# Performance work log

Measured on AMD Instinct MI355X. Metric: run time of the kernel, lower is better.

Reference implementation:

```python
import jax, jax.numpy as jnp
import numpy as np

T, S, B, D, H, F, E = 1024, 1024, 4, 1024, 16, 4096, 8
HD = D // H
N = T * B                      # tokens entering MoE
CAP = 2 * N // E               # top-2 capacity per expert


def setup_inputs() -> dict:
    key = jax.random.key(0)
    ks = jax.random.split(key, 16)
    sc = 0.02
    rn = lambda k, shp, s=sc: jax.random.normal(k, shp, jnp.float32) * s
    return {
        "tgt": jax.random.normal(ks[0], (T, B, D), jnp.float32),
        "memory": jax.random.normal(ks[1], (S, B, D), jnp.float32),
        "sa_in_w": rn(ks[2], (3 * D, D)), "sa_in_b": jnp.zeros((3 * D,), jnp.float32),
        "sa_out_w": rn(ks[3], (D, D)), "sa_out_b": jnp.zeros((D,), jnp.float32),
        "ca_in_w": rn(ks[4], (3 * D, D)), "ca_in_b": jnp.zeros((3 * D,), jnp.float32),
        "ca_out_w": rn(ks[5], (D, D)), "ca_out_b": jnp.zeros((D,), jnp.float32),
        "ln1_g": jnp.ones((D,), jnp.float32), "ln1_b": jnp.zeros((D,), jnp.float32),
        "ln2_g": jnp.ones((D,), jnp.float32), "ln2_b": jnp.zeros((D,), jnp.float32),
        "ln3_g": jnp.ones((D,), jnp.float32), "ln3_b": jnp.zeros((D,), jnp.float32),
        "wg": rn(ks[6], (D, E)),
        "w1": rn(ks[7], (E, D, F)), "b1": jnp.zeros((E, F), jnp.float32),
        "w2": rn(ks[8], (E, F, D)), "b2": jnp.zeros((E, D), jnp.float32),
    }


def layer_norm(x, g, b, eps=1e-5):
    mu = jnp.mean(x, axis=-1, keepdims=True)
    var = jnp.var(x, axis=-1, keepdims=True)
    return (x - mu) * jax.lax.rsqrt(var + eps) * g + b


def mha(q_in, k_in, v_in, in_w, in_b, out_w, out_b):
    # q_in: [Tq,B,D], k_in/v_in: [Tk,B,D]; torch MultiheadAttention math (eval)
    wq, wk, wv = jnp.split(in_w, 3, axis=0)
    bq, bk, bv = jnp.split(in_b, 3)
    def heads(x, w, bias):
        y = x @ w.T + bias                       # [Tx,B,D]
        return y.reshape(x.shape[0], B, H, HD).transpose(1, 2, 0, 3)  # [B,H,Tx,hd]
    q, k, v = heads(q_in, wq, bq), heads(k_in, wk, bk), heads(v_in, wv, bv)
    scores = jnp.einsum('bhtd,bhsd->bhts', q, k) / np.sqrt(HD)
    attn = jax.nn.softmax(scores, axis=-1)
    o = jnp.einsum('bhts,bhsd->bhtd', attn, v)   # [B,H,Tq,hd]
    o = o.transpose(2, 0, 1, 3).reshape(q_in.shape[0], B, D)
    return o @ out_w.T + out_b


def moe_top2(x, wg, w1, b1, w2, b2):
    # x: [N,D]. Top-2 gating with capacity dispatch + grouped expert FFN.
    logits = x @ wg                               # [N,E]
    gates = jax.nn.softmax(logits, axis=-1)
    idx1 = jnp.argmax(gates, axis=-1)             # [N]
    m1 = jax.nn.one_hot(idx1, E, dtype=x.dtype)   # [N,E]
    gates_wo1 = jnp.where(m1 > 0, -jnp.inf, logits)
    idx2 = jnp.argmax(gates_wo1, axis=-1)
    m2 = jax.nn.one_hot(idx2, E, dtype=x.dtype)
    ar = jnp.arange(N)
    g1 = gates[ar, idx1]
    g2 = gates[ar, idx2]
    denom = g1 + g2 + 1e-9
    g1, g2 = g1 / denom, g2 / denom
    # positions within each expert buffer (first-come-first-serve, top1 before top2)
    pos1 = jnp.cumsum(m1, axis=0)[ar, idx1] - 1
    counts1 = jnp.sum(m1, axis=0)                 # [E]
    pos2 = jnp.cumsum(m2, axis=0)[ar, idx2] - 1 + counts1[idx2]
    keep1 = (pos1 < CAP).astype(x.dtype)
    keep2 = (pos2 < CAP).astype(x.dtype)
    p1 = jnp.clip(pos1, 0, CAP - 1).astype(jnp.int32)
    p2 = jnp.clip(pos2, 0, CAP - 1).astype(jnp.int32)
    buf = jnp.zeros((E, CAP, D), x.dtype)
    buf = buf.at[idx1, p1].add(x * keep1[:, None])
    buf = buf.at[idx2, p2].add(x * keep2[:, None])
    # grouped expert FFN: [E,CAP,D] -> [E,CAP,F] -> [E,CAP,D]
    h = jax.nn.relu(jnp.einsum('ecd,edf->ecf', buf, w1) + b1[:, None, :])
    eo = jnp.einsum('ecf,efd->ecd', h, w2) + b2[:, None, :]
    out = eo[idx1, p1] * (g1 * keep1)[:, None] + eo[idx2, p2] * (g2 * keep2)[:, None]
    return out


def reference(tgt, memory, sa_in_w, sa_in_b, sa_out_w, sa_out_b,
              ca_in_w, ca_in_b, ca_out_w, ca_out_b,
              ln1_g, ln1_b, ln2_g, ln2_b, ln3_g, ln3_b,
              wg, w1, b1, w2, b2):
    t2 = mha(tgt, tgt, tgt, sa_in_w, sa_in_b, sa_out_w, sa_out_b)
    x = layer_norm(tgt + t2, ln1_g, ln1_b)
    t2 = mha(x, memory, memory, ca_in_w, ca_in_b, ca_out_w, ca_out_b)
    x = layer_norm(x + t2, ln2_g, ln2_b)
    m = moe_top2(x.reshape(N, D), wg, w1, b1, w2, b2).reshape(T, B, D)
    x = layer_norm(x + m, ln3_g, ln3_b)
    return x
```

## Files before the change

### kernel.cpp

```cpp
#include <hip/hip_runtime.h>
#include <hip/hip_bf16.h>


typedef __bf16 bf16;
typedef __bf16 bf16x2 __attribute__((ext_vector_type(2)));
typedef __bf16 bf16x4 __attribute__((ext_vector_type(4)));
typedef __bf16 bf16x8 __attribute__((ext_vector_type(8)));
typedef float  f32x4  __attribute__((ext_vector_type(4)));

static_assert(sizeof(bf16) == 2, "bf16 size");

#define CAP_ 1024

#define GLOAD16(g, l)                                                  \
  __builtin_amdgcn_global_load_lds(                                    \
      (const __attribute__((address_space(1))) unsigned int*)(g),      \
      (__attribute__((address_space(3))) unsigned int*)(l), 16, 0, 0)

#define BAR() do { asm volatile("" ::: "memory"); __builtin_amdgcn_s_barrier(); asm volatile("" ::: "memory"); } while (0)

static const long OFF_WSAIN  = 0L;
static const long OFF_WSAOUT = 6291456L;
static const long OFF_WCAIN  = 8388608L;
static const long OFF_WCAOUT = 14680064L;
static const long OFF_BTGT   = 16777216L;
static const long OFF_BMEM   = 25165824L;
static const long OFF_QKV    = 33554432L;
static const long OFF_QS     = OFF_QKV;
static const long OFF_KS     = OFF_QKV + 8388608L;
static const long OFF_VS     = OFF_QKV + 16777216L;
static const long OFF_EO1    = 33554432L;
static const long OFF_VT     = 58720256L;
static const long OFF_AO     = 67108864L;
static const long OFF_PROJ   = 75497472L;
static const long OFF_X1     = 92274688L;
static const long OFF_X2     = 109051904L;
static const long OFF_SCORES = 125829120L;
static const long OFF_H      = OFF_SCORES + 67108864L;
static const long OFF_GATE   = 260046848L;
static const long OFF_E1   = OFF_GATE;
static const long OFF_E2   = OFF_GATE + 16384L;
static const long OFF_G1   = OFF_GATE + 32768L;
static const long OFF_G2   = OFF_GATE + 49152L;
static const long OFF_D1   = OFF_GATE + 65536L;
static const long OFF_D2   = OFF_GATE + 81920L;
static const long OFF_S1   = OFF_GATE + 98304L;
static const long OFF_S2   = OFF_GATE + 114688L;

__device__ __forceinline__ int xcd_swz(int bid, int nwg) {
  int q = nwg >> 3, r = nwg & 7;
  int xcd = bid & 7, idx = bid >> 3;
  return (xcd < r ? xcd * (q + 1) : r * (q + 1) + (xcd - r) * q) + idx;
}

__global__ __launch_bounds__(256) void k_cvt6(
    const float* __restrict__ s0, const float* __restrict__ s1,
    const float* __restrict__ s2, const float* __restrict__ s3,
    const float* __restrict__ s4, const float* __restrict__ s5,
    bf16* __restrict__ d0, bf16* __restrict__ d1, bf16* __restrict__ d2,
    bf16* __restrict__ d3, bf16* __restrict__ d4, bf16* __restrict__ d5) {
  long b = blockIdx.x;
  const float* s; bf16* d; long off;
  if (b < 3072)       { s = s0; d = d0; off = b; }
  else if (b < 4096)  { s = s1; d = d1; off = b - 3072; }
  else if (b < 7168)  { s = s2; d = d2; off = b - 4096; }
  else if (b < 8192)  { s = s3; d = d3; off = b - 7168; }
  else if (b < 12288) { s = s4; d = d4; off = b - 8192; }
  else                { s = s5; d = d5; off = b - 12288; }
  long i = off * 256 + threadIdx.x;
  float4 v = ((const float4*)s)[i];
  bf16x4 o = {(bf16)v.x, (bf16)v.y, (bf16)v.z, (bf16)v.w};
  ((bf16x4*)d)[i] = o;
}

__global__ __launch_bounds__(256) void k_transpose_f32_bf16(const float* __restrict__ in,
                                                            bf16* __restrict__ out, int R, int C) {
  __shared__ float t[64][66];
  int z = blockIdx.z;
  long r0 = (long)blockIdx.y * 64, c0 = (long)blockIdx.x * 64;
  const float* ib = in + (long)z * R * C;
  bf16* ob = out + (long)z * R * C;
  int tid = threadIdx.x;
  int x = tid & 15, y = tid >> 4;
  #pragma unroll
  for (int j = 0; j < 4; j++) {
    int sr = y + j * 16;
    float4 v = *(const float4*)&ib[(r0 + sr) * C + c0 + x * 4];
    t[sr][x * 4 + 0] = v.x; t[sr][x * 4 + 1] = v.y;
    t[sr][x * 4 + 2] = v.z; t[sr][x * 4 + 3] = v.w;
  }
  __syncthreads();
  int xs = tid & 7, jj = tid >> 3;
  #pragma unroll
  for (int p = 0; p < 2; p++) {
    int c = jj + p * 32;
    bf16x8 o;
    #pragma unroll
    for (int k = 0; k < 8; k++) o[k] = (bf16)t[xs * 8 + k][c];
    *(bf16x8*)&ob[(c0 + c) * R + r0 + xs * 8] = o;
  }
}

__global__ __launch_bounds__(256) void k_extract_vt(const bf16* __restrict__ in,
                                                    bf16* __restrict__ out) {
  __shared__ bf16 t[64][68];
  const int bh = blockIdx.y;
  const long r0 = (long)blockIdx.x * 64;
  const int b = bh >> 4, h = bh & 15;
  const bf16* ib = in + (long)b * 1048576 + h * 64;
  bf16* ob = out + (long)bh * 65536;
  int tid = threadIdx.x;
  int x = tid & 15, y = tid >> 4;
  #pragma unroll
  for (int j = 0; j < 4; j++) {
    int sr = y + j * 16;
    *(bf16x4*)&t[sr][x * 4] = *(const bf16x4*)&ib[(r0 + sr) * 1024 + x * 4];
  }
  __syncthreads();
  #pragma unroll
  for (int p = 0; p < 4; p++) {
    int c = y + p * 16;
    bf16x4 o = {t[x * 4 + 0][c], t[x * 4 + 1][c], t[x * 4 + 2][c], t[x * 4 + 3][c]};
    *(bf16x4*)&ob[(long)c * 1024 + r0 + x * 4] = o;
  }
}

template <int BM, int BN, int WM, int WN, bool RELU, bool PERM, typename OutT>
__global__ __launch_bounds__(256) void k_gemm_nt(
    const bf16* __restrict__ A, const bf16* __restrict__ Bp,
    OutT* __restrict__ C, const float* __restrict__ bias,
    int K, long lda, long ldb, long ldc, float alpha, int zdiv,
    long sA1, long sA0, long sB1, long sB0, long sC1, long sC0,
    long sBias1, long sBias0) {
  constexpr int BK = 32;
  constexpr int WTM = BM / WM, WTN = BN / WN, MR = WTM / 16, NR = WTN / 16;
  constexpr int AISS = BM * BK / 2048;
  constexpr int BISS = BN * BK / 2048;
  __shared__ bf16 sa[BM * BK];
  __shared__ bf16 sb[BN * BK];
  const int nwg = gridDim.x * gridDim.y * gridDim.z;
  const int bid = blockIdx.x + gridDim.x * (blockIdx.y + gridDim.y * blockIdx.z);
  const int lid = xcd_swz(bid, nwg);
  const int bx = lid % gridDim.x;
  const int rem = lid / gridDim.x;
  const int by = rem % gridDim.y;
  const int z = rem / gridDim.y;
  const int zh = z / zdiv, zl = z - zh * zdiv;
  const bf16* Ab = A + zh * sA1 + zl * sA0 + (long)by * BM * lda;
  const bf16* Bb = Bp + zh * sB1 + zl * sB0 + (long)bx * BN * ldb;
  const int tid = threadIdx.x, lane = tid & 63, wid = tid >> 6;
  const int wm = wid / WN, wn = wid % WN;

  const int srow = tid >> 2;
  const int scol = (tid & 3) * 8;
  const bf16* aptr[AISS];
  bf16* aldst[AISS];
  #pragma unroll
  for (int i = 0; i < AISS; i++) {
    aptr[i] = Ab + (long)(srow + i * 64) * lda + scol;
    aldst[i] = &sa[i * 2048 + (wid << 9)];
  }
  const bf16* bptr[BISS];
  bf16* bldst[BISS];
  #pragma unroll
  for (int i = 0; i < BISS; i++) {
    bptr[i] = Bb + (long)(srow + i * 64) * ldb + scol;
    bldst[i] = &sb[i * 2048 + (wid << 9)];
  }

  f32x4 acc[MR][NR] = {};
  const int rA = wm * WTM + (lane & 15);
  const int rB = wn * WTN + (lane & 15);
  const int kk = (lane >> 4) * 8;

  for (int k0 = 0; k0 < K; k0 += BK) {
    #pragma unroll
    for (int i = 0; i < AISS; i++) GLOAD16(aptr[i] + k0, aldst[i]);
    #pragma unroll
    for (int i = 0; i < BISS; i++) GLOAD16(bptr[i] + k0, bldst[i]);
    __syncthreads();
    bf16x8 af[MR], bfr[NR];
    #pragma unroll
    for (int mi = 0; mi < MR; mi++) af[mi] = *(const bf16x8*)&sa[(rA + mi * 16) * BK + kk];
    #pragma unroll
    for (int ni = 0; ni < NR; ni++) bfr[ni] = *(const bf16x8*)&sb[(rB + ni * 16) * BK + kk];
    #pragma unroll
    for (int mi = 0; mi < MR; mi++)
      #pragma unroll
      for (int ni = 0; ni < NR; ni++)
        acc[mi][ni] = __builtin_amdgcn_mfma_f32_16x16x32_bf16(af[mi], bfr[ni], acc[mi][ni], 0, 0, 0);
    __syncthreads();
  }
  OutT* Cb = C + zh * sC1 + zl * sC0;
  const float* biasb = bias ? (bias + zh * sBias1 + zl * sBias0) : nullptr;
  const long rowBase = (long)by * BM + wm * WTM + ((lane >> 4) * 4);
  const long colBase = (long)bx * BN + wn * WTN + (lane & 15);
  #pragma unroll
  for (int mi = 0; mi < MR; mi++) {
    #pragma unroll
    for (int ni = 0; ni < NR; ni++) {
      long col = colBase + ni * 16;
      float bv = biasb ? biasb[col] : 0.f;
      #pragma unroll
      for (int r = 0; r < 4; r++) {
        long row = rowBase + mi * 16 + r;
        long prow = PERM ? ((row & 3) * 1024 + (row >> 2)) : row;
        float v = acc[mi][ni][r] * alpha + bv;
        if (RELU) v = fmaxf(v, 0.f);
        Cb[prow * ldc + col] = (OutT)v;
      }
    }
  }
}

template <bool RELU, bool PERM, typename OutT>
__global__ __launch_bounds__(512, 2) void k_gemm8p(
    const bf16* __restrict__ A, const bf16* __restrict__ Bp,
    OutT* __restrict__ C, const float* __restrict__ bias,
    int K, long lda, long ldb, long ldc, int zdiv,
    long sA1, long sA0, long sB1, long sB0, long sC1, long sC0, long sBias1) {
  __shared__ bf16 smem[65536];
  const int nwg = gridDim.x * gridDim.y * gridDim.z;
  const int bid = blockIdx.x + gridDim.x * (blockIdx.y + gridDim.y * blockIdx.z);
  const int lid = xcd_swz(bid, nwg);
  const int bx = lid % gridDim.x;
  const int rem = lid / gridDim.x;
  const int by = rem % gridDim.y;
  const int z = rem / gridDim.y;
  const int zh = z / zdiv, zl = z - zh * zdiv;
  const bf16* Ab = A + zh * sA1 + zl * sA0 + (long)by * 256 * lda;
  const bf16* Bb = Bp + zh * sB1 + zl * sB0 + (long)bx * 256 * ldb;
  const int tid = threadIdx.x, lane = tid & 63, wid = tid >> 6;
  const int wm = wid >> 2, wn = wid & 3;
  const int lane15 = lane & 15, grp = lane >> 4;
  const int s_r = (wid << 3) + (lane >> 3);
  const int s_k = ((lane & 7) ^ (lane >> 3)) << 3;
  const int ldst = wid << 9;
  const int in0 = (grp << 4) ^ ((lane & 7) << 4);
  const int in1 = (64 | (grp << 4)) ^ ((lane & 7) << 4);

  const int NT = K >> 6;
  f32x4 acc[8][4] = {};
  bf16x8 a[4][2], b[2][2][2];

  const bf16* pA0 = Ab + (long)s_r * lda + s_k;
  const bf16* pB0 = Bb + (long)s_r * ldb + s_k;

  auto stageA = [&](int q, long koff, int cb) {
    GLOAD16(pA0 + (long)(q << 6) * lda + koff, &smem[cb + (q << 12) + ldst]);
  };
  auto stageB = [&](int q, long koff, int cb) {
    GLOAD16(pB0 + (long)(q << 6) * ldb + koff, &smem[cb + 16384 + (q << 12) + ldst]);
  };
  auto loadA_ks = [&](int mh, int ks, int cb) {
    const int inx = ks ? in1 : in0;
    #pragma unroll
    for (int mi2 = 0; mi2 < 4; mi2++) {
      int r = wm * 128 + mh * 64 + mi2 * 16 + lane15;
      a[mi2][ks] = *(const bf16x8*)&smem[cb + (r << 6) + (inx >> 1)];
    }
  };
  auto loadB_ks = [&](int nh, int ks, int cb) {
    const int inx = ks ? in1 : in0;
    #pragma unroll
    for (int ni2 = 0; ni2 < 2; ni2++) {
      int c = wn * 64 + nh * 32 + ni2 * 16 + lane15;
      b[nh][ni2][ks] = *(const bf16x8*)&smem[cb + 16384 + (c << 6) + (inx >> 1)];
    }
  };
  auto mfmaQ = [&](int mh, int nh) {
    __builtin_amdgcn_s_setprio(1);
    #pragma unroll
    for (int ks = 0; ks < 2; ks++)
      #pragma unroll
      for (int mi2 = 0; mi2 < 4; mi2++)
        #pragma unroll
        for (int ni2 = 0; ni2 < 2; ni2++)
          acc[mh * 4 + mi2][nh * 2 + ni2] = __builtin_amdgcn_mfma_f32_16x16x32_bf16(
              a[mi2][ks], b[nh][ni2][ks], acc[mh * 4 + mi2][nh * 2 + ni2], 0, 0, 0);
    __builtin_amdgcn_s_setprio(0);
  };

  #pragma unroll
  for (int q = 0; q < 4; q++) { stageA(q, 0, 0); stageB(q, 0, 0); }
  #pragma unroll
  for (int q = 0; q < 4; q++) { stageA(q, 64, 32768); stageB(q, 64, 32768); }
  asm volatile("s_waitcnt vmcnt(8)" ::: "memory");
  BAR();
  loadB_ks(0, 0, 0);
  loadB_ks(0, 1, 0);

  long koff = 128;
  for (int t = 0; t < NT; t++) {
    const int cb = (t & 1) << 15;
    const bool dostage = (t + 2) < NT;
    const bool doread = (t + 1) < NT;
    loadA_ks(0, 0, cb);
    BAR();
    loadA_ks(0, 1, cb);
    loadB_ks(1, 0, cb);
    loadB_ks(1, 1, cb);
    mfmaQ(0, 0);
    BAR();
    if (dostage) { stageA(0, koff, cb); stageA(2, koff, cb); }
    BAR();
    mfmaQ(0, 1);
    BAR();
    loadA_ks(1, 0, cb);
    if (dostage) {
      stageB(0, koff, cb); stageB(1, koff, cb);
      stageB(2, koff, cb); stageB(3, koff, cb);
    }
    BAR();
    loadA_ks(1, 1, cb);
    mfmaQ(1, 0);
    BAR();
    if (dostage) {
      stageA(1, koff, cb); stageA(3, koff, cb);
      asm volatile("s_waitcnt vmcnt(8)" ::: "memory");
    } else if (doread) {
      asm volatile("s_waitcnt vmcnt(0)" ::: "memory");
    }
    BAR();
    if (doread) {
      loadB_ks(0, 0, cb ^ 32768);
      loadB_ks(0, 1, cb ^ 32768);
    }
    mfmaQ(1, 1);
    BAR();
    koff += 64;
  }

  OutT* Cb = C + zh * sC1 + zl * sC0;
  const float* biasb = bias ? (bias + zh * sBias1) : nullptr;
  float bv[4];
  #pragma unroll
  for (int ni = 0; ni < 4; ni++)
    bv[ni] = biasb ? biasb[(long)bx * 256 + wn * 64 + ni * 16 + lane15] : 0.f;
  const long rowBase = (long)by * 256 + wm * 128 + grp * 4;
  const long colBase = (long)bx * 256 + wn * 64 + lane15;
  #pragma unroll
  for (int mi = 0; mi < 8; mi++) {
    #pragma unroll
    for (int ni = 0; ni < 4; ni++) {
      long col = colBase + ni * 16;
      #pragma unroll
      for (int r = 0; r < 4; r++) {
        long row = rowBase + mi * 16 + r;
        long prow = PERM ? ((row & 3) * 1024 + (row >> 2)) : row;
        float v = acc[mi][ni][r] + bv[ni];
        if (RELU) v = fmaxf(v, 0.f);
        Cb[prow * ldc + col] = (OutT)v;
      }
    }
  }
}

__global__ __launch_bounds__(256) void k_flash(
    const bf16* __restrict__ q, const bf16* __restrict__ kk,
    const bf16* __restrict__ vt, bf16* __restrict__ ao) {
  __shared__ bf16 kt[2][2048];
  __shared__ bf16 vtt[2][2048];
  __shared__ bf16 p_lds[4][32 * 72];
  const int nwg = gridDim.x * gridDim.y;
  const int bid = blockIdx.x + gridDim.x * blockIdx.y;
  const int lid = xcd_swz(bid, nwg);
  const int qt = lid & 7;
  const int bh = lid >> 3;
  const int b = bh >> 4, h = bh & 15;
  const int tid = threadIdx.x, lane = tid & 63, wid = tid >> 6;
  const int colLane = lane & 15, grp = lane >> 4;
  const bf16* qb = q + (long)b * 1048576 + h * 64;
  const bf16* kb = kk + (long)b * 1048576 + h * 64;
  const bf16* vb = vt + (long)bh * 65536;

  bf16x8 qf[2][2];
  const int qrow0 = qt * 128 + wid * 32 + colLane;
  #pragma unroll
  for (int mi = 0; mi < 2; mi++)
    #pragma unroll
    for (int ks = 0; ks < 2; ks++)
      qf[mi][ks] = *(const bf16x8*)&qb[(long)(qrow0 + mi * 16) * 1024 + ks * 32 + grp * 8];

  const int srow = tid >> 2;
  const int scol = (tid & 3) * 8;

  f32x4 oacc[2][4] = {};
  float m_[2][4], l_[2][4];
  #pragma unroll
  for (int mi = 0; mi < 2; mi++)
    #pragma unroll
    for (int r = 0; r < 4; r++) { m_[mi][r] = -INFINITY; l_[mi][r] = 0.f; }
  bf16* pl = &p_lds[wid][0];

  for (int s0 = 0; s0 < 1024; s0 += 64) {
    GLOAD16(&kb[(long)(s0 + srow) * 1024 + scol], &kt[0][wid << 9]);
    GLOAD16(&kb[(long)(s0 + srow) * 1024 + 32 + scol], &kt[1][wid << 9]);
    GLOAD16(&vb[(long)srow * 1024 + s0 + scol], &vtt[0][wid << 9]);
    GLOAD16(&vb[(long)srow * 1024 + s0 + 32 + scol], &vtt[1][wid << 9]);
    __syncthreads();

    f32x4 sacc[2][4] = {};
    bf16x8 kf[4][2];
    #pragma unroll
    for (int ni = 0; ni < 4; ni++)
      #pragma unroll
      for (int ks = 0; ks < 2; ks++)
        kf[ni][ks] = *(const bf16x8*)&kt[ks][(colLane + ni * 16) * 32 + grp * 8];
    #pragma unroll
    for (int ks = 0; ks < 2; ks++)
      #pragma unroll
      for (int mi = 0; mi < 2; mi++)
        #pragma unroll
        for (int ni = 0; ni < 4; ni++)
          sacc[mi][ni] = __builtin_amdgcn_mfma_f32_16x16x32_bf16(qf[mi][ks], kf[ni][ks], sacc[mi][ni], 0, 0, 0);

    float mnew[2][4], sc[2][4], psum[2][4];
    #pragma unroll
    for (int mi = 0; mi < 2; mi++)
      #pragma unroll
      for (int r = 0; r < 4; r++) {
        float vx = fmaxf(fmaxf(sacc[mi][0][r], sacc[mi][1][r]),
                         fmaxf(sacc[mi][2][r], sacc[mi][3][r])) * 0.125f;
        #pragma unroll
        for (int o = 1; o < 16; o <<= 1) vx = fmaxf(vx, __shfl_xor(vx, o));
        float mn = fmaxf(m_[mi][r], vx);
        sc[mi][r] = __expf(m_[mi][r] - mn);
        m_[mi][r] = mn; mnew[mi][r] = mn;
        l_[mi][r] *= sc[mi][r];
        psum[mi][r] = 0.f;
      }
    #pragma unroll
    for (int mi = 0; mi < 2; mi++)
      #pragma unroll
      for (int ni = 0; ni < 4; ni++)
        #pragma unroll
        for (int r = 0; r < 4; r++)
          oacc[mi][ni][r] *= sc[mi][r];
    #pragma unroll
    for (int mi = 0; mi < 2; mi++)
      #pragma unroll
      for (int ni = 0; ni < 4; ni++)
        #pragma unroll
        for (int r = 0; r < 4; r++) {
          float p = __expf(sacc[mi][ni][r] * 0.125f - mnew[mi][r]);
          psum[mi][r] += p;
          pl[(mi * 16 + grp * 4 + r) * 72 + ni * 16 + colLane] = (bf16)p;
        }
    #pragma unroll
    for (int mi = 0; mi < 2; mi++)
      #pragma unroll
      for (int r = 0; r < 4; r++) {
        float ps = psum[mi][r];
        #pragma unroll
        for (int o = 1; o < 16; o <<= 1) ps += __shfl_xor(ps, o);
        l_[mi][r] += ps;
      }

    bf16x8 pa[2][2], vf[4][2];
    #pragma unroll
    for (int mi = 0; mi < 2; mi++)
      #pragma unroll
      for (int ks = 0; ks < 2; ks++)
        pa[mi][ks] = *(const bf16x8*)&pl[(colLane + mi * 16) * 72 + ks * 32 + grp * 8];
    #pragma unroll
    for (int ni = 0; ni < 4; ni++)
      #pragma unroll
      for (int ks = 0; ks < 2; ks++)
        vf[ni][ks] = *(const bf16x8*)&vtt[ks][(colLane + ni * 16) * 32 + grp * 8];
    #pragma unroll
    for (int ks = 0; ks < 2; ks++)
      #pragma unroll
      for (int mi = 0; mi < 2; mi++)
        #pragma unroll
        for (int ni = 0; ni < 4; ni++)
          oacc[mi][ni] = __builtin_amdgcn_mfma_f32_16x16x32_bf16(pa[mi][ks], vf[ni][ks], oacc[mi][ni], 0, 0, 0);
    __syncthreads();
  }

  #pragma unroll
  for (int mi = 0; mi < 2; mi++)
    #pragma unroll
    for (int r = 0; r < 4; r++) {
      float inv = 1.f / l_[mi][r];
      int t = qt * 128 + wid * 32 + mi * 16 + grp * 4 + r;
      long n = (long)t * 4 + b;
      #pragma unroll
      for (int ni = 0; ni < 4; ni++)
        ao[n * 1024 + h * 64 + ni * 16 + colLane] = (bf16)(oacc[mi][ni][r] * inv);
    }
}

__global__ __launch_bounds__(256) void k_add_ln(const float* __restrict__ a, const float* __restrict__ b,
                                                const float* __restrict__ g, const float* __restrict__ be,
                                                float* __restrict__ out, bf16* __restrict__ outb) {
  long row = blockIdx.x;
  int tid = threadIdx.x;
  float4 va = ((const float4*)(a + row * 1024))[tid];
  float4 vb = ((const float4*)(b + row * 1024))[tid];
  float v[4] = {va.x + vb.x, va.y + vb.y, va.z + vb.z, va.w + vb.w};
  float s = v[0] + v[1] + v[2] + v[3];
  float sq = v[0] * v[0] + v[1] * v[1] + v[2] * v[2] + v[3] * v[3];
  #pragma unroll
  for (int o = 32; o; o >>= 1) { s += __shfl_xor(s, o); sq += __shfl_xor(sq, o); }
  __shared__ float r1[4], r2[4];
  int wid = tid >> 6;
  if ((tid & 63) == 0) { r1[wid] = s; r2[wid] = sq; }
  __syncthreads();
  s = r1[0] + r1[1] + r1[2] + r1[3];
  sq = r2[0] + r2[1] + r2[2] + r2[3];
  float mu = s * (1.f / 1024.f);
  float var = sq * (1.f / 1024.f) - mu * mu;
  float rstd = rsqrtf(var + 1e-5f);
  float4 vg = ((const float4*)g)[tid];
  float4 vbe = ((const float4*)be)[tid];
  float y0 = (v[0] - mu) * rstd * vg.x + vbe.x;
  float y1 = (v[1] - mu) * rstd * vg.y + vbe.y;
  float y2 = (v[2] - mu) * rstd * vg.z + vbe.z;
  float y3 = (v[3] - mu) * rstd * vg.w + vbe.w;
  ((float4*)(out + row * 1024))[tid] = make_float4(y0, y1, y2, y3);
  if (outb) {
    bf16x4 o = {(bf16)y0, (bf16)y1, (bf16)y2, (bf16)y3};
    ((bf16x4*)(outb + row * 1024))[tid] = o;
  }
}

__global__ __launch_bounds__(256) void k_add_ln_gate(
    const float* __restrict__ a, const float* __restrict__ b,
    const float* __restrict__ g, const float* __restrict__ be,
    const float* __restrict__ wg, float* __restrict__ out,
    int* __restrict__ e1, int* __restrict__ e2,
    float* __restrict__ g1, float* __restrict__ g2) {
  long row = blockIdx.x;
  int tid = threadIdx.x;
  float4 va = ((const float4*)(a + row * 1024))[tid];
  float4 vb = ((const float4*)(b + row * 1024))[tid];
  float v[4] = {va.x + vb.x, va.y + vb.y, va.z + vb.z, va.w + vb.w};
  float s = v[0] + v[1] + v[2] + v[3];
  float sq = v[0] * v[0] + v[1] * v[1] + v[2] * v[2] + v[3] * v[3];
  #pragma unroll
  for (int o = 32; o; o >>= 1) { s += __shfl_xor(s, o); sq += __shfl_xor(sq, o); }
  __shared__ float r1[4], r2[4];
  __shared__ float gred[4][8];
  int wid = tid >> 6, lane = tid & 63;
  if (lane == 0) { r1[wid] = s; r2[wid] = sq; }
  __syncthreads();
  s = r1[0] + r1[1] + r1[2] + r1[3];
  sq = r2[0] + r2[1] + r2[2] + r2[3];
  float mu = s * (1.f / 1024.f);
  float var = sq * (1.f / 1024.f) - mu * mu;
  float rstd = rsqrtf(var + 1e-5f);
  float4 vg = ((const float4*)g)[tid];
  float4 vbe = ((const float4*)be)[tid];
  float y[4];
  y[0] = (v[0] - mu) * rstd * vg.x + vbe.x;
  y[1] = (v[1] - mu) * rstd * vg.y + vbe.y;
  y[2] = (v[2] - mu) * rstd * vg.z + vbe.z;
  y[3] = (v[3] - mu) * rstd * vg.w + vbe.w;
  ((float4*)(out + row * 1024))[tid] = make_float4(y[0], y[1], y[2], y[3]);
  float acc[8] = {0.f, 0.f, 0.f, 0.f, 0.f, 0.f, 0.f, 0.f};
  const float* wr = wg + (long)tid * 32;
  #pragma unroll
  for (int j = 0; j < 4; j++) {
    float4 w0 = *(const float4*)(wr + j * 8);
    float4 w1 = *(const float4*)(wr + j * 8 + 4);
    acc[0] += y[j] * w0.x; acc[1] += y[j] * w0.y; acc[2] += y[j] * w0.z; acc[3] += y[j] * w0.w;
    acc[4] += y[j] * w1.x; acc[5] += y[j] * w1.y; acc[6] += y[j] * w1.z; acc[7] += y[j] * w1.w;
  }
  #pragma unroll
  for (int e = 0; e < 8; e++)
    #pragma unroll
    for (int o = 32; o; o >>= 1) acc[e] += __shfl_xor(acc[e], o);
  if (lane == 0) {
    #pragma unroll
    for (int e = 0; e < 8; e++) gred[wid][e] = acc[e];
  }
  __syncthreads();
  if (tid == 0) {
    float L[8];
    #pragma unroll
    for (int e = 0; e < 8; e++) L[e] = gred[0][e] + gred[1][e] + gred[2][e] + gred[3][e];
    int i1 = 0; float b1v = L[0];
    #pragma unroll
    for (int e = 1; e < 8; e++) if (L[e] > b1v) { b1v = L[e]; i1 = e; }
    int i2 = -1; float b2v = -INFINITY;
    #pragma unroll
    for (int e = 0; e < 8; e++) if (e != i1 && L[e] > b2v) { b2v = L[e]; i2 = e; }
    float den = 0.f;
    #pragma unroll
    for (int e = 0; e < 8; e++) den += __expf(L[e] - b1v);
    float gg1 = 1.f / den;
    float gg2 = __expf(b2v - b1v) / den;
    float dn = gg1 + gg2 + 1e-9f;
    e1[row] = i1; e2[row] = i2; g1[row] = gg1 / dn; g2[row] = gg2 / dn;
  }
}

__global__ __launch_bounds__(256) void k_positions(const int* __restrict__ e1, const int* __restrict__ e2,
                                                   const float* __restrict__ g1, const float* __restrict__ g2,
                                                   int* __restrict__ d1, int* __restrict__ d2,
                                                   float* __restrict__ s1, float* __restrict__ s2) {
  const int e = blockIdx.x;
  const int tid = threadIdx.x, lane = tid & 63, wid = tid >> 6;
  __shared__ int wsum[4];
  int f[16];
  int cnt = 0;
  #pragma unroll
  for (int i = 0; i < 16; i++) { f[i] = (e1[tid * 16 + i] == e) ? 1 : 0; cnt += f[i]; }
  int inc = cnt;
  #pragma unroll
  for (int o = 1; o < 64; o <<= 1) { int v = __shfl_up(inc, o); if (lane >= o) inc += v; }
  if (lane == 63) wsum[wid] = inc;
  __syncthreads();
  int base = inc - cnt;
  for (int w = 0; w < wid; w++) base += wsum[w];
  const int total1 = wsum[0] + wsum[1] + wsum[2] + wsum[3];
  int run = base;
  #pragma unroll
  for (int i = 0; i < 16; i++) {
    int n = tid * 16 + i;
    if (f[i]) {
      int p = run++;
      d1[n] = e * CAP_ + (p < CAP_ ? p : CAP_ - 1);
      s1[n] = (p < CAP_) ? g1[n] : 0.f;
    }
  }
  cnt = 0;
  #pragma unroll
  for (int i = 0; i < 16; i++) { f[i] = (e2[tid * 16 + i] == e) ? 1 : 0; cnt += f[i]; }
  inc = cnt;
  #pragma unroll
  for (int o = 1; o < 64; o <<= 1) { int v = __shfl_up(inc, o); if (lane >= o) inc += v; }
  __syncthreads();
  if (lane == 63) wsum[wid] = inc;
  __syncthreads();
  base = inc - cnt + total1;
  for (int w = 0; w < wid; w++) base += wsum[w];
  run = base;
  #pragma unroll
  for (int i = 0; i < 16; i++) {
    int n = tid * 16 + i;
    if (f[i]) {
      int p = run++;
      d2[n] = e * CAP_ + (p < CAP_ ? p : CAP_ - 1);
      s2[n] = (p < CAP_) ? g2[n] : 0.f;
    }
  }
}

__global__ __launch_bounds__(256) void k_scatter(const float* __restrict__ x, const int* __restrict__ d1,
                                                 const int* __restrict__ d2, const float* __restrict__ s1,
                                                 const float* __restrict__ s2, bf16* __restrict__ buf) {
  int n = blockIdx.x;
  int tid = threadIdx.x;
  float4 v = ((const float4*)(x + (long)n * 1024))[tid];
  bf16x4 o = {(bf16)v.x, (bf16)v.y, (bf16)v.z, (bf16)v.w};
  if (s1[n] != 0.f) ((bf16x4*)(buf + (long)d1[n] * 1024))[tid] = o;
  if (s2[n] != 0.f) ((bf16x4*)(buf + (long)d2[n] * 1024))[tid] = o;
}

__global__ __launch_bounds__(256) void k_gather_ln(const float* __restrict__ x,
                                                   const bf16* __restrict__ p0, const bf16* __restrict__ p1,
                                                   const float* __restrict__ b2,
                                                   const int* __restrict__ d1, const int* __restrict__ d2,
                                                   const float* __restrict__ s1, const float* __restrict__ s2,
                                                   const float* __restrict__ g, const float* __restrict__ be,
                                                   float* __restrict__ out) {
  long n = blockIdx.x;
  int tid = threadIdx.x;
  float a1 = s1[n], a2 = s2[n];
  long i1 = (long)d1[n] * 1024, i2 = (long)d2[n] * 1024;
  long e1b = (long)(d1[n] >> 10) * 1024, e2b = (long)(d2[n] >> 10) * 1024;
  float4 vx = ((const float4*)(x + n * 1024))[tid];
  bf16x4 q10 = *(const bf16x4*)&p0[i1 + tid * 4];
  bf16x4 q11 = *(const bf16x4*)&p1[i1 + tid * 4];
  bf16x4 q20 = *(const bf16x4*)&p0[i2 + tid * 4];
  bf16x4 q21 = *(const bf16x4*)&p1[i2 + tid * 4];
  float4 vb1 = ((const float4*)(b2 + e1b))[tid];
  float4 vb2 = ((const float4*)(b2 + e2b))[tid];
  float v[4];
  float xs[4] = {vx.x, vx.y, vx.z, vx.w};
  float b1a[4] = {vb1.x, vb1.y, vb1.z, vb1.w};
  float b2a[4] = {vb2.x, vb2.y, vb2.z, vb2.w};
  float s = 0.f, sq = 0.f;
  #pragma unroll
  for (int i = 0; i < 4; i++) {
    float r1v = (float)q10[i] + (float)q11[i] + b1a[i];
    float r2v = (float)q20[i] + (float)q21[i] + b2a[i];
    float y = xs[i] + a1 * r1v + a2 * r2v;
    v[i] = y; s += y; sq += y * y;
  }
  #pragma unroll
  for (int o = 32; o; o >>= 1) { s += __shfl_xor(s, o); sq += __shfl_xor(sq, o); }
  __shared__ float r1[4], r2[4];
  int wid = tid >> 6;
  if ((tid & 63) == 0) { r1[wid] = s; r2[wid] = sq; }
  __syncthreads();
  s = r1[0] + r1[1] + r1[2] + r1[3];
  sq = r2[0] + r2[1] + r2[2] + r2[3];
  float mu = s * (1.f / 1024.f);
  float var = sq * (1.f / 1024.f) - mu * mu;
  float rstd = rsqrtf(var + 1e-5f);
  float4 vg = ((const float4*)g)[tid];
  float4 vbe = ((const float4*)be)[tid];
  float ga[4] = {vg.x, vg.y, vg.z, vg.w};
  float ba[4] = {vbe.x, vbe.y, vbe.z, vbe.w};
  float4 o;
  o.x = (v[0] - mu) * rstd * ga[0] + ba[0];
  o.y = (v[1] - mu) * rstd * ga[1] + ba[1];
  o.z = (v[2] - mu) * rstd * ga[2] + ba[2];
  o.w = (v[3] - mu) * rstd * ga[3] + ba[3];
  ((float4*)(out + n * 1024))[tid] = o;
}

extern "C" void kernel_launch(void* const* d_in, const int* in_sizes, int n_in,
                              void* d_out, int out_size, void* d_ws, size_t ws_size,
                              hipStream_t stream) {
  const float* tgt      = (const float*)d_in[0];
  const float* memory   = (const float*)d_in[1];
  const float* sa_in_w  = (const float*)d_in[2];
  const float* sa_in_b  = (const float*)d_in[3];
  const float* sa_out_w = (const float*)d_in[4];
  const float* sa_out_b = (const float*)d_in[5];
  const float* ca_in_w  = (const float*)d_in[6];
  const float* ca_in_b  = (const float*)d_in[7];
  const float* ca_out_w = (const float*)d_in[8];
  const float* ca_out_b = (const float*)d_in[9];
  const float* ln1_g    = (const float*)d_in[10];
  const float* ln1_b    = (const float*)d_in[11];
  const float* ln2_g    = (const float*)d_in[12];
  const float* ln2_b    = (const float*)d_in[13];
  const float* ln3_g    = (const float*)d_in[14];
  const float* ln3_b    = (const float*)d_in[15];
  const float* wg       = (const float*)d_in[16];
  const float* w1       = (const float*)d_in[17];
  const float* b1       = (const float*)d_in[18];
  const float* w2       = (const float*)d_in[19];
  const float* b2       = (const float*)d_in[20];

  char* ws = (char*)d_ws;
  auto B16 = [&](long o) { return (bf16*)(ws + o); };
  auto F32 = [&](long o) { return (float*)(ws + o); };
  auto I32 = [&](long o) { return (int*)(ws + o); };

  const dim3 blk256(256), blk512(512);

  k_cvt6<<<16384, blk256, 0, stream>>>(sa_in_w, sa_out_w, ca_in_w, ca_out_w, tgt, memory,
                                       B16(OFF_WSAIN), B16(OFF_WSAOUT), B16(OFF_WCAIN),
                                       B16(OFF_WCAOUT), B16(OFF_BTGT), B16(OFF_BMEM));

  k_gemm8p<false, true, bf16><<<dim3(4, 16, 3), blk512, 0, stream>>>(
      B16(OFF_BTGT), B16(OFF_WSAIN), B16(OFF_QS), sa_in_b,
      1024, 1024, 1024, 1024, 1,
      0, 0, 1048576, 0, 4194304, 0, 1024);
  k_extract_vt<<<dim3(16, 64), blk256, 0, stream>>>(B16(OFF_VS), B16(OFF_VT));
  k_flash<<<dim3(8, 64), blk256, 0, stream>>>(B16(OFF_QS), B16(OFF_KS), B16(OFF_VT), B16(OFF_AO));
  k_gemm_nt<128, 64, 4, 1, false, false, float><<<dim3(16, 32, 1), blk256, 0, stream>>>(
      B16(OFF_AO), B16(OFF_WSAOUT), F32(OFF_PROJ), sa_out_b,
      1024, 1024, 1024, 1024, 1.f, 1, 0, 0, 0, 0, 0, 0, 0, 0);
  k_add_ln<<<4096, blk256, 0, stream>>>(tgt, F32(OFF_PROJ), ln1_g, ln1_b, F32(OFF_X1), B16(OFF_BTGT));

  k_gemm_nt<128, 64, 4, 1, false, true, bf16><<<dim3(16, 32, 3), blk256, 0, stream>>>(
      B16(OFF_BTGT), B16(OFF_WCAIN), B16(OFF_QS), ca_in_b,
      1024, 1024, 1024, 1024, 1.f, 2,
      4194304, 4194304, 2097152, 1048576, 8388608, 4194304, 2048, 1024);
  k_extract_vt<<<dim3(16, 64), blk256, 0, stream>>>(B16(OFF_VS), B16(OFF_VT));
  k_flash<<<dim3(8, 64), blk256, 0, stream>>>(B16(OFF_QS), B16(OFF_KS), B16(OFF_VT), B16(OFF_AO));
  k_gemm_nt<128, 64, 4, 1, false, false, float><<<dim3(16, 32, 1), blk256, 0, stream>>>(
      B16(OFF_AO), B16(OFF_WCAOUT), F32(OFF_PROJ), ca_out_b,
      1024, 1024, 1024, 1024, 1.f, 1, 0, 0, 0, 0, 0, 0, 0, 0);
  k_add_ln_gate<<<4096, blk256, 0, stream>>>(F32(OFF_X1), F32(OFF_PROJ), ln2_g, ln2_b, wg,
                                             F32(OFF_X2), I32(OFF_E1), I32(OFF_E2),
                                             F32(OFF_G1), F32(OFF_G2));

  k_positions<<<8, blk256, 0, stream>>>(I32(OFF_E1), I32(OFF_E2), F32(OFF_G1), F32(OFF_G2),
                                        I32(OFF_D1), I32(OFF_D2), F32(OFF_S1), F32(OFF_S2));
  k_scatter<<<4096, blk256, 0, stream>>>(F32(OFF_X2), I32(OFF_D1), I32(OFF_D2),
                                         F32(OFF_S1), F32(OFF_S2), B16(OFF_QKV));
  k_transpose_f32_bf16<<<dim3(64, 16, 8), blk256, 0, stream>>>(w1, B16(OFF_SCORES), 1024, 4096);
  k_gemm8p<true, false, bf16><<<dim3(16, 4, 8), blk512, 0, stream>>>(
      B16(OFF_QKV), B16(OFF_SCORES), B16(OFF_H), b1,
      1024, 1024, 1024, 4096, 1,
      1048576, 0, 4194304, 0, 4194304, 0, 4096);
  k_transpose_f32_bf16<<<dim3(16, 64, 8), blk256, 0, stream>>>(w2, B16(OFF_SCORES), 4096, 1024);
  k_gemm8p<false, false, bf16><<<dim3(4, 4, 16), blk512, 0, stream>>>(
      B16(OFF_H), B16(OFF_SCORES), B16(OFF_PROJ), nullptr,
      2048, 4096, 4096, 1024, 2,
      4194304, 2048, 4194304, 2048, 1048576, (OFF_EO1 - OFF_PROJ) / 2, 0);
  k_gather_ln<<<4096, blk256, 0, stream>>>(F32(OFF_X2), B16(OFF_PROJ), B16(OFF_EO1), b2,
                                           I32(OFF_D1), I32(OFF_D2),
                                           F32(OFF_S1), F32(OFF_S2), ln3_g, ln3_b, (float*)d_out);

  (void)in_sizes; (void)n_in; (void)out_size; (void)ws_size;
}
```

Measured before the change: 550.3 us.

## Add single-buffered 256x256 GEMM variant with higher occupancy for expert FFN1

Adds a new GEMM kernel for the first expert FFN matmul. It loads each K tile into one 64KB shared-memory buffer and reads it back through split A/B fragment loads, with MFMA issued at raised priority. Launch bounds of 4 waves per SIMD are meant to let more workgroups overlap loads with compute, replacing the previous software-pipelined kernel. The cost is that loads no longer overlap compute inside a workgroup, which may expose memory latency if occupancy does not hide it.

```diff
diff --git a/kernel.cpp b/kernel.cpp
--- a/kernel.cpp
+++ b/kernel.cpp
@@ -356,6 +356,108 @@
   }
 }
 
+template <bool RELU, typename OutT>
+__global__ __launch_bounds__(512, 4) void k_gemm2b(
+    const bf16* __restrict__ A, const bf16* __restrict__ Bp,
+    OutT* __restrict__ C, const float* __restrict__ bias,
+    int K, long lda, long ldb, long ldc, int zdiv,
+    long sA1, long sA0, long sB1, long sB0, long sC1, long sC0, long sBias1) {
+  __shared__ bf16 smem[32768];
+  const int nwg = gridDim.x * gridDim.y * gridDim.z;
+  const int bid = blockIdx.x + gridDim.x * (blockIdx.y + gridDim.y * blockIdx.z);
+  const int lid = xcd_swz(bid, nwg);
+  const int bx = lid % gridDim.x;
+  const int rem = lid / gridDim.x;
+  const int by = rem % gridDim.y;
+  const int z = rem / gridDim.y;
+  const int zh = z / zdiv, zl = z - zh * zdiv;
+  const bf16* Ab = A + zh * sA1 + zl * sA0 + (long)by * 256 * lda;
+  const bf16* Bb = Bp + zh * sB1 + zl * sB0 + (long)bx * 256 * ldb;
+  const int tid = threadIdx.x, lane = tid & 63, wid = tid >> 6;
+  const int wm = wid >> 2, wn = wid & 3;
+  const int lane15 = lane & 15, grp = lane >> 4;
+  const int s_r = (wid << 3) + (lane >> 3);
+  const int s_k = ((lane & 7) ^ (lane >> 3)) << 3;
+  const int ldst = wid << 9;
+  const int in0 = (grp << 4) ^ ((lane & 7) << 4);
+  const int in1 = (64 | (grp << 4)) ^ ((lane & 7) << 4);
+
+  const int NT = K >> 6;
+  f32x4 acc[8][4] = {};
+  bf16x8 a[4][2], b[2][2][2];
+
+  const bf16* pA0 = Ab + (long)s_r * lda + s_k;
+  const bf16* pB0 = Bb + (long)s_r * ldb + s_k;
+
+  auto loadA = [&](int mh) {
+    #pragma unroll
+    for (int mi2 = 0; mi2 < 4; mi2++) {
+      int r = wm * 128 + mh * 64 + mi2 * 16 + lane15;
+      a[mi2][0] = *(const bf16x8*)&smem[(r << 6) + (in0 >> 1)];
+      a[mi2][1] = *(const bf16x8*)&smem[(r << 6) + (in1 >> 1)];
+    }
+  };
+  auto loadB = [&](int nh) {
+    #pragma unroll
+    for (int ni2 = 0; ni2 < 2; ni2++) {
+      int c = wn * 64 + nh * 32 + ni2 * 16 + lane15;
+      b[nh][ni2][0] = *(const bf16x8*)&smem[16384 + (c << 6) + (in0 >> 1)];
+      b[nh][ni2][1] = *(const bf16x8*)&smem[16384 + (c << 6) + (in1 >> 1)];
+    }
+  };
+  auto mfmaQ = [&](int mh, int nh) {
+    __builtin_amdgcn_s_setprio(1);
+    #pragma unroll
+    for (int ks = 0; ks < 2; ks++)
+      #pragma unroll
+      for (int mi2 = 0; mi2 < 4; mi2++)
+        #pragma unroll
+        for (int ni2 = 0; ni2 < 2; ni2++)
+          acc[mh * 4 + mi2][nh * 2 + ni2] = __builtin_amdgcn_mfma_f32_16x16x32_bf16(
+              a[mi2][ks], b[nh][ni2][ks], acc[mh * 4 + mi2][nh * 2 + ni2], 0, 0, 0);
+    __builtin_amdgcn_s_setprio(0);
+  };
+
+  long koff = 0;
+  for (int t = 0; t < NT; t++) {
+    #pragma unroll
+    for (int q = 0; q < 4; q++) {
+      GLOAD16(pA0 + (long)(q << 6) * lda + koff, &smem[(q << 12) + ldst]);
+      GLOAD16(pB0 + (long)(q << 6) * ldb + koff, &smem[16384 + (q << 12) + ldst]);
+    }
+    __syncthreads();
+    loadA(0); loadB(0); loadB(1);
+    mfmaQ(0, 0); mfmaQ(0, 1);
+    loadA(1);
+    mfmaQ(1, 0); mfmaQ(1, 1);
+    __syncthreads();
+    koff += 64;
+  }
+
+  OutT* Cb = C + zh * sC1 + zl * sC0;
+  const float* biasb = bias ? (bias + zh * sBias1) : nullptr;
+  float bv[4];
+  #pragma unroll
+  for (int ni = 0; ni < 4; ni++)
+    bv[ni] = biasb ? biasb[(long)bx * 256 + wn * 64 + ni * 16 + lane15] : 0.f;
+  const long rowBase = (long)by * 256 + wm * 128 + grp * 4;
+  const long colBase = (long)bx * 256 + wn * 64 + lane15;
+  #pragma unroll
+  for (int mi = 0; mi < 8; mi++) {
+    #pragma unroll
+    for (int ni = 0; ni < 4; ni++) {
+      long col = colBase + ni * 16;
+      #pragma unroll
+      for (int r = 0; r < 4; r++) {
+        long row = rowBase + mi * 16 + r;
+        float v = acc[mi][ni][r] + bv[ni];
+        if (RELU) v = fmaxf(v, 0.f);
+        Cb[row * ldc + col] = (OutT)v;
+      }
+    }
+  }
+}
+
 __global__ __launch_bounds__(256) void k_flash(
     const bf16* __restrict__ q, const bf16* __restrict__ kk,
     const bf16* __restrict__ vt, bf16* __restrict__ ao) {
@@ -778,7 +880,7 @@
   k_scatter<<<4096, blk256, 0, stream>>>(F32(OFF_X2), I32(OFF_D1), I32(OFF_D2),
                                          F32(OFF_S1), F32(OFF_S2), B16(OFF_QKV));
   k_transpose_f32_bf16<<<dim3(64, 16, 8), blk256, 0, stream>>>(w1, B16(OFF_SCORES), 1024, 4096);
-  k_gemm8p<true, false, bf16><<<dim3(16, 4, 8), blk512, 0, stream>>>(
+  k_gemm2b<true, bf16><<<dim3(16, 4, 8), blk512, 0, stream>>>(
       B16(OFF_QKV), B16(OFF_SCORES), B16(OFF_H), b1,
       1024, 1024, 1024, 4096, 1,
       1048576, 0, 4194304, 0, 4194304, 0, 4096);
```

New measurement: 1.114 ms. 2.02x slower.
